# Kernel optimization log

Measured on AMD Instinct MI355X. Metric: run time of the kernel, lower is better.

The kernel has to match this reference:

```python
import jax, jax.numpy as jnp
import numpy as np

N_NODES = 50000
N_EDGES = 800000
IN_DIM = 64
HID = 128
OUT_DIM = 128
N_LAYERS = 3
LN_EPS = 1e-5


def setup_inputs() -> dict:
    key = jax.random.key(0)
    ks = jax.random.split(key, 12)
    x = jax.random.normal(ks[0], (N_NODES, IN_DIM), dtype=jnp.float32)
    edge_index = jax.random.randint(ks[1], (2, N_EDGES), 0, N_NODES, dtype=jnp.int32)
    # parameters
    W_in = jax.random.normal(ks[2], (IN_DIM, HID), dtype=jnp.float32) / np.sqrt(IN_DIM)
    b_in = jnp.zeros((HID,), dtype=jnp.float32)
    W_layers = jax.random.normal(ks[3], (N_LAYERS, HID, HID), dtype=jnp.float32) / np.sqrt(HID)
    b_layers = jnp.zeros((N_LAYERS, HID), dtype=jnp.float32)
    ln_g = jnp.ones((N_LAYERS, HID), dtype=jnp.float32)
    ln_b = jnp.zeros((N_LAYERS, HID), dtype=jnp.float32)
    W_out = jax.random.normal(ks[4], (HID, OUT_DIM), dtype=jnp.float32) / np.sqrt(HID)
    b_out = jnp.zeros((OUT_DIM,), dtype=jnp.float32)
    return {
        "x": x, "edge_index": edge_index, "num_nodes_actual": 48000,
        "W_in": W_in, "b_in": b_in,
        "W_layers": W_layers, "b_layers": b_layers,
        "ln_g": ln_g, "ln_b": ln_b,
        "W_out": W_out, "b_out": b_out,
    }


def _layer_norm(h, g, b):
    mu = jnp.mean(h, axis=-1, keepdims=True)
    var = jnp.mean(jnp.square(h - mu), axis=-1, keepdims=True)
    return (h - mu) * jax.lax.rsqrt(var + LN_EPS) * g + b


def reference(x, edge_index, num_nodes_actual, W_in, b_in, W_layers, b_layers, ln_g, ln_b, W_out, b_out):
    n = x.shape[0]
    src, dst = edge_index[0], edge_index[1]
    # degree-normalized scatter-add aggregation (same for all layers)
    degree = jax.ops.segment_sum(jnp.ones_like(src, dtype=x.dtype), dst, num_segments=n)
    inv_deg = 1.0 / jnp.clip(degree, 1.0)[:, None]  # [N,1]

    h = x @ W_in + b_in  # [N, HID]
    for i in range(N_LAYERS):
        residual = h
        agg = jax.ops.segment_sum(h[src], dst, num_segments=n) * inv_deg
        h = (h + agg) @ W_layers[i] + b_layers[i]
        h = _layer_norm(h, ln_g[i], ln_b[i])
        h = jax.nn.relu(h)
        h = h + residual
    h = h @ W_out + b_out  # [N, OUT_DIM]
    # mean over actual (non-padding) nodes, keepdim
    return jnp.mean(h[:num_nodes_actual], axis=0, keepdims=True)  # [1, OUT_DIM]
```

## Files before the change

kernel.cpp:

```cpp
#include <hip/hip_runtime.h>

#define HID 128
#define INP 64
#define LN_EPS 1e-5f
#define RT 64

typedef __attribute__((ext_vector_type(8))) short bf16x8;
typedef __attribute__((ext_vector_type(4))) float f32x4;

__device__ __forceinline__ unsigned f2bf(float f) {
    unsigned u = __float_as_uint(f);
    return (u + 0x7FFFu + ((u >> 16) & 1u)) >> 16;
}
__device__ __forceinline__ float bflo(unsigned v) { return __uint_as_float(v << 16); }
__device__ __forceinline__ float bfhi(unsigned v) { return __uint_as_float(v & 0xFFFF0000u); }

__global__ __launch_bounds__(256) void k_count(const int* __restrict__ dst, int nE, int* __restrict__ cnt,
                                               int* __restrict__ rank, int nEdgeThreads,
                                               const float* __restrict__ W_in, const float* __restrict__ W_l,
                                               unsigned short* __restrict__ Wt_in, unsigned short* __restrict__ Wt_l) {
    int t = blockIdx.x * 256 + threadIdx.x;
    if (t < nEdgeThreads) {
        int base = t * 16;
        if (base + 16 <= nE) {
            int4 d[4];
#pragma unroll
            for (int j = 0; j < 4; ++j) d[j] = *reinterpret_cast<const int4*>(dst + base + j * 4);
            int p[16];
#pragma unroll
            for (int j = 0; j < 4; ++j) {
                p[j * 4 + 0] = atomicAdd(&cnt[d[j].x], 1);
                p[j * 4 + 1] = atomicAdd(&cnt[d[j].y], 1);
                p[j * 4 + 2] = atomicAdd(&cnt[d[j].z], 1);
                p[j * 4 + 3] = atomicAdd(&cnt[d[j].w], 1);
            }
#pragma unroll
            for (int j = 0; j < 4; ++j)
                *reinterpret_cast<int4*>(rank + base + j * 4) =
                    make_int4(p[j * 4 + 0], p[j * 4 + 1], p[j * 4 + 2], p[j * 4 + 3]);
        } else {
            for (int e = base; e < nE; ++e) rank[e] = atomicAdd(&cnt[dst[e]], 1);
        }
        return;
    }
    int i = t - nEdgeThreads;
    if (i < 128 * 64) {
        int col = i >> 6, k = i & 63;
        Wt_in[i] = (unsigned short)f2bf(W_in[(size_t)k * HID + col]);
    } else if (i < 128 * 64 + 3 * 128 * 128) {
        int j = i - 128 * 64;
        int l = j >> 14, r = j & 16383;
        int col = r >> 7, k = r & 127;
        Wt_l[j] = (unsigned short)f2bf(W_l[(size_t)l * 16384 + (size_t)k * HID + col]);
    }
}

__global__ void k_scan1(const int* __restrict__ cnt, int n, int* __restrict__ rowp, int* __restrict__ bsum) {
    __shared__ int s[256];
    int i = blockIdx.x * 256 + threadIdx.x;
    int v = (i < n) ? cnt[i] : 0;
    s[threadIdx.x] = v;
    __syncthreads();
    for (int off = 1; off < 256; off <<= 1) {
        int t = (threadIdx.x >= off) ? s[threadIdx.x - off] : 0;
        __syncthreads();
        s[threadIdx.x] += t;
        __syncthreads();
    }
    if (i < n) rowp[i] = s[threadIdx.x] - v;
    if (threadIdx.x == 255) bsum[blockIdx.x] = s[255];
}

__global__ void k_scan3(int* __restrict__ rowp, const int* __restrict__ bsum, const int* __restrict__ cnt,
                        int n, int nE, float* __restrict__ invd, int nb) {
    __shared__ int s[256];
    __shared__ int boff;
    int v = (threadIdx.x < nb) ? bsum[threadIdx.x] : 0;
    s[threadIdx.x] = v;
    __syncthreads();
    for (int off = 1; off < 256; off <<= 1) {
        int t = (threadIdx.x >= off) ? s[threadIdx.x - off] : 0;
        __syncthreads();
        s[threadIdx.x] += t;
        __syncthreads();
    }
    if (threadIdx.x == blockIdx.x) boff = s[threadIdx.x] - v;
    __syncthreads();
    int i = blockIdx.x * 256 + threadIdx.x;
    if (i < n) {
        rowp[i] += boff;
        int c = cnt[i];
        invd[i] = 1.0f / (float)(c > 1 ? c : 1);
    } else if (i == n) {
        rowp[n] = nE;
    }
}

__global__ __launch_bounds__(256) void k_fillproj(const float* __restrict__ x,
                                                  const unsigned short* __restrict__ Wt,
                                                  const float* __restrict__ b,
                                                  unsigned* __restrict__ hout, int n, int tgrid,
                                                  const int* __restrict__ src, const int* __restrict__ dst,
                                                  const int* __restrict__ rank, const int* __restrict__ rowp,
                                                  int nE, int* __restrict__ csrc) {
    const int tid = threadIdx.x;
    if (blockIdx.x >= tgrid) {
        int t = (blockIdx.x - tgrid) * 256 + tid;
        int base = t * 16;
        if (base + 16 <= nE) {
            int4 d[4], s[4], r[4];
#pragma unroll
            for (int j = 0; j < 4; ++j) {
                d[j] = *reinterpret_cast<const int4*>(dst + base + j * 4);
                s[j] = *reinterpret_cast<const int4*>(src + base + j * 4);
                r[j] = *reinterpret_cast<const int4*>(rank + base + j * 4);
            }
#pragma unroll
            for (int j = 0; j < 4; ++j) {
                __builtin_nontemporal_store(s[j].x, &csrc[rowp[d[j].x] + r[j].x]);
                __builtin_nontemporal_store(s[j].y, &csrc[rowp[d[j].y] + r[j].y]);
                __builtin_nontemporal_store(s[j].z, &csrc[rowp[d[j].z] + r[j].z]);
                __builtin_nontemporal_store(s[j].w, &csrc[rowp[d[j].w] + r[j].w]);
            }
        } else if (base < nE) {
            for (int e = base; e < nE; ++e)
                __builtin_nontemporal_store(src[e], &csrc[rowp[dst[e]] + rank[e]]);
        }
        return;
    }
    __shared__ unsigned short xs[RT * INP];
    const int row0 = blockIdx.x * RT;
#pragma unroll
    for (int j = 0; j < 2; ++j) {
        int fid = tid + j * 256;
        int r = fid >> 3, c = fid & 7;
        int grow = row0 + r;
        unsigned o[4] = {0, 0, 0, 0};
        if (grow < n) {
            float4 v0 = *reinterpret_cast<const float4*>(x + (size_t)grow * INP + c * 8);
            float4 v1 = *reinterpret_cast<const float4*>(x + (size_t)grow * INP + c * 8 + 4);
            o[0] = f2bf(v0.x) | (f2bf(v0.y) << 16);
            o[1] = f2bf(v0.z) | (f2bf(v0.w) << 16);
            o[2] = f2bf(v1.x) | (f2bf(v1.y) << 16);
            o[3] = f2bf(v1.z) | (f2bf(v1.w) << 16);
        }
        int sw = c ^ (r & 7);
        *reinterpret_cast<uint4*>(xs + r * INP + sw * 8) = make_uint4(o[0], o[1], o[2], o[3]);
    }
    __syncthreads();

    const int l = tid & 63;
    const int w = tid >> 6;
    const int l15 = l & 15, lg = l >> 4;
    const int xrow = w * 16 + l15;

    f32x4 acc[8];
#pragma unroll
    for (int t = 0; t < 8; ++t) acc[t] = (f32x4){0.f, 0.f, 0.f, 0.f};

#pragma unroll
    for (int kc = 0; kc < 2; ++kc) {
        int bc = (kc * 4 + lg) ^ (xrow & 7);
        bf16x8 bfrag = *reinterpret_cast<const bf16x8*>(xs + xrow * INP + bc * 8);
        const unsigned short* wp = Wt + (size_t)l15 * INP + kc * 32 + lg * 8;
        bf16x8 af[8];
#pragma unroll
        for (int t = 0; t < 8; ++t) af[t] = *reinterpret_cast<const bf16x8*>(wp + (size_t)t * 16 * INP);
#pragma unroll
        for (int t = 0; t < 8; ++t)
            acc[t] = __builtin_amdgcn_mfma_f32_16x16x32_bf16(af[t], bfrag, acc[t], 0, 0, 0);
    }

    int grow = row0 + xrow;
    if (grow < n) {
#pragma unroll
        for (int t = 0; t < 8; ++t) {
            int c0 = t * 16 + lg * 4;
            f32x4 bb = *reinterpret_cast<const f32x4*>(b + c0);
            f32x4 o = acc[t] + bb;
            uint2 p;
            p.x = f2bf(o.x) | (f2bf(o.y) << 16);
            p.y = f2bf(o.z) | (f2bf(o.w) << 16);
            *reinterpret_cast<uint2*>(hout + (size_t)grow * 64 + t * 8 + lg * 2) = p;
        }
    }
}

__global__ __launch_bounds__(256) void k_agg(const unsigned* __restrict__ hb, const int* __restrict__ rowp,
                                             const int* __restrict__ csrc, const float* __restrict__ invd,
                                             unsigned* __restrict__ aggx, int n) {
    int node = blockIdx.x * 4 + (threadIdx.x >> 6);
    if (node >= n) return;
    int lane = threadIdx.x & 63;
    int grp = lane >> 4, cidx = lane & 15;
    int e0 = rowp[node], e1 = rowp[node + 1];
    int deg = e1 - e0;
    const uint4* hb4 = reinterpret_cast<const uint4*>(hb);
    float a0 = 0, a1 = 0, a2 = 0, a3 = 0, a4 = 0, a5 = 0, a6 = 0, a7 = 0;

    for (int base = 0; base < deg; base += 64) {
        int m = deg - base;
        if (m > 64) m = 64;
        int myidx = (base + lane < deg) ? csrc[e0 + base + lane] : 0;
        int steps = (m + 3) >> 2;
        int jj = 0;
        for (; jj + 4 <= steps; jj += 4) {
            uint4 v[4];
#pragma unroll
            for (int k = 0; k < 4; ++k) {
                int ei = (jj + k) * 4 + grp;
                int s = __shfl(myidx, ei);
                v[k] = (ei < m) ? hb4[(size_t)s * 16 + cidx] : make_uint4(0, 0, 0, 0);
            }
#pragma unroll
            for (int k = 0; k < 4; ++k) {
                a0 += bflo(v[k].x); a1 += bfhi(v[k].x);
                a2 += bflo(v[k].y); a3 += bfhi(v[k].y);
                a4 += bflo(v[k].z); a5 += bfhi(v[k].z);
                a6 += bflo(v[k].w); a7 += bfhi(v[k].w);
            }
        }
        for (; jj < steps; ++jj) {
            int ei = jj * 4 + grp;
            int s = __shfl(myidx, ei);
            if (ei < m) {
                uint4 v = hb4[(size_t)s * 16 + cidx];
                a0 += bflo(v.x); a1 += bfhi(v.x);
                a2 += bflo(v.y); a3 += bfhi(v.y);
                a4 += bflo(v.z); a5 += bfhi(v.z);
                a6 += bflo(v.w); a7 += bfhi(v.w);
            }
        }
    }
    a0 += __shfl_xor(a0, 16, 64); a0 += __shfl_xor(a0, 32, 64);
    a1 += __shfl_xor(a1, 16, 64); a1 += __shfl_xor(a1, 32, 64);
    a2 += __shfl_xor(a2, 16, 64); a2 += __shfl_xor(a2, 32, 64);
    a3 += __shfl_xor(a3, 16, 64); a3 += __shfl_xor(a3, 32, 64);
    a4 += __shfl_xor(a4, 16, 64); a4 += __shfl_xor(a4, 32, 64);
    a5 += __shfl_xor(a5, 16, 64); a5 += __shfl_xor(a5, 32, 64);
    a6 += __shfl_xor(a6, 16, 64); a6 += __shfl_xor(a6, 32, 64);
    a7 += __shfl_xor(a7, 16, 64); a7 += __shfl_xor(a7, 32, 64);

    if (grp == 0) {
        float inv = invd[node];
        uint4 self = hb4[(size_t)node * 16 + cidx];
        unsigned o0 = f2bf(bflo(self.x) + a0 * inv) | (f2bf(bfhi(self.x) + a1 * inv) << 16);
        unsigned o1 = f2bf(bflo(self.y) + a2 * inv) | (f2bf(bfhi(self.y) + a3 * inv) << 16);
        unsigned o2 = f2bf(bflo(self.z) + a4 * inv) | (f2bf(bfhi(self.z) + a5 * inv) << 16);
        unsigned o3 = f2bf(bflo(self.w) + a6 * inv) | (f2bf(bfhi(self.w) + a7 * inv) << 16);
        int sw = cidx ^ (node & 7);
        *reinterpret_cast<uint4*>(aggx + (size_t)node * 64 + sw * 4) = make_uint4(o0, o1, o2, o3);
    }
}

__global__ __launch_bounds__(256) void k_layer(const unsigned* __restrict__ hin,
                                               unsigned* __restrict__ hout,
                                               const unsigned* __restrict__ aggx,
                                               const unsigned short* __restrict__ Wt,
                                               const float* __restrict__ bias, const float* __restrict__ g,
                                               const float* __restrict__ lnb, int n) {
    const int tid = threadIdx.x;
    const int row0 = blockIdx.x * RT;
    const int lane = tid & 63;
    const int w = tid >> 6;
    const int l15 = lane & 15, lg = lane >> 4;
    const int xrow = w * 16 + l15;
    const int grow = row0 + xrow;

    const unsigned short* xg = reinterpret_cast<const unsigned short*>(aggx) + (size_t)grow * HID;

    f32x4 acc[8];
#pragma unroll
    for (int t = 0; t < 8; ++t) acc[t] = (f32x4){0.f, 0.f, 0.f, 0.f};

#pragma unroll
    for (int kc = 0; kc < 4; ++kc) {
        int bc = (kc * 4 + lg) ^ (xrow & 7);
        bf16x8 bfrag = *reinterpret_cast<const bf16x8*>(xg + bc * 8);
        const unsigned short* wp = Wt + (size_t)l15 * HID + kc * 32 + lg * 8;
        bf16x8 af[8];
#pragma unroll
        for (int t = 0; t < 8; ++t) af[t] = *reinterpret_cast<const bf16x8*>(wp + (size_t)t * 16 * HID);
#pragma unroll
        for (int t = 0; t < 8; ++t)
            acc[t] = __builtin_amdgcn_mfma_f32_16x16x32_bf16(af[t], bfrag, acc[t], 0, 0, 0);
    }

    float s = 0.f, q = 0.f;
#pragma unroll
    for (int t = 0; t < 8; ++t) {
        int c0 = t * 16 + lg * 4;
        f32x4 bb = *reinterpret_cast<const f32x4*>(bias + c0);
        acc[t] = acc[t] + bb;
        s += acc[t].x + acc[t].y + acc[t].z + acc[t].w;
        q += acc[t].x * acc[t].x + acc[t].y * acc[t].y + acc[t].z * acc[t].z + acc[t].w * acc[t].w;
    }
    s += __shfl_xor(s, 16, 64);
    s += __shfl_xor(s, 32, 64);
    q += __shfl_xor(q, 16, 64);
    q += __shfl_xor(q, 32, 64);
    float mu = s * (1.0f / HID);
    float var = q * (1.0f / HID) - mu * mu;
    float rs = rsqrtf(var + LN_EPS);

    if (grow < n) {
#pragma unroll
        for (int t = 0; t < 8; ++t) {
            int c0 = t * 16 + lg * 4;
            uint2 rv = *reinterpret_cast<const uint2*>(hin + (size_t)grow * 64 + t * 8 + lg * 2);
            f32x4 gv = *reinterpret_cast<const f32x4*>(g + c0);
            f32x4 lb = *reinterpret_cast<const f32x4*>(lnb + c0);
            float o0 = fmaxf((acc[t].x - mu) * rs * gv.x + lb.x, 0.f) + bflo(rv.x);
            float o1 = fmaxf((acc[t].y - mu) * rs * gv.y + lb.y, 0.f) + bfhi(rv.x);
            float o2 = fmaxf((acc[t].z - mu) * rs * gv.z + lb.z, 0.f) + bflo(rv.y);
            float o3 = fmaxf((acc[t].w - mu) * rs * gv.w + lb.w, 0.f) + bfhi(rv.y);
            uint2 p;
            p.x = f2bf(o0) | (f2bf(o1) << 16);
            p.y = f2bf(o2) | (f2bf(o3) << 16);
            *reinterpret_cast<uint2*>(hout + (size_t)grow * 64 + t * 8 + lg * 2) = p;
        }
    }
}

__global__ __launch_bounds__(256) void k_layerF(const unsigned* __restrict__ hin,
                                                const unsigned* __restrict__ aggx,
                                                const unsigned short* __restrict__ Wt,
                                                const float* __restrict__ bias, const float* __restrict__ g,
                                                const float* __restrict__ lnb,
                                                const int* __restrict__ n_act_p,
                                                float* __restrict__ accum) {
    __shared__ float red[4][4][8][4];
    const int tid = threadIdx.x;
    const int row0 = blockIdx.x * RT;
    const int lane = tid & 63;
    const int w = tid >> 6;
    const int l15 = lane & 15, lg = lane >> 4;
    const int xrow = w * 16 + l15;
    const int grow = row0 + xrow;
    const int na = *n_act_p;

    const unsigned short* xg = reinterpret_cast<const unsigned short*>(aggx) + (size_t)grow * HID;

    f32x4 acc[8];
#pragma unroll
    for (int t = 0; t < 8; ++t) acc[t] = (f32x4){0.f, 0.f, 0.f, 0.f};

#pragma unroll
    for (int kc = 0; kc < 4; ++kc) {
        int bc = (kc * 4 + lg) ^ (xrow & 7);
        bf16x8 bfrag = *reinterpret_cast<const bf16x8*>(xg + bc * 8);
        const unsigned short* wp = Wt + (size_t)l15 * HID + kc * 32 + lg * 8;
        bf16x8 af[8];
#pragma unroll
        for (int t = 0; t < 8; ++t) af[t] = *reinterpret_cast<const bf16x8*>(wp + (size_t)t * 16 * HID);
#pragma unroll
        for (int t = 0; t < 8; ++t)
            acc[t] = __builtin_amdgcn_mfma_f32_16x16x32_bf16(af[t], bfrag, acc[t], 0, 0, 0);
    }

    float s = 0.f, q = 0.f;
#pragma unroll
    for (int t = 0; t < 8; ++t) {
        int c0 = t * 16 + lg * 4;
        f32x4 bb = *reinterpret_cast<const f32x4*>(bias + c0);
        acc[t] = acc[t] + bb;
        s += acc[t].x + acc[t].y + acc[t].z + acc[t].w;
        q += acc[t].x * acc[t].x + acc[t].y * acc[t].y + acc[t].z * acc[t].z + acc[t].w * acc[t].w;
    }
    s += __shfl_xor(s, 16, 64);
    s += __shfl_xor(s, 32, 64);
    q += __shfl_xor(q, 16, 64);
    q += __shfl_xor(q, 32, 64);
    float mu = s * (1.0f / HID);
    float var = q * (1.0f / HID) - mu * mu;
    float rs = rsqrtf(var + LN_EPS);

    const float msk = (grow < na) ? 1.f : 0.f;
#pragma unroll
    for (int t = 0; t < 8; ++t) {
        int c0 = t * 16 + lg * 4;
        uint2 rv = *reinterpret_cast<const uint2*>(hin + (size_t)grow * 64 + t * 8 + lg * 2);
        f32x4 gv = *reinterpret_cast<const f32x4*>(g + c0);
        f32x4 lb = *reinterpret_cast<const f32x4*>(lnb + c0);
        float o0 = (fmaxf((acc[t].x - mu) * rs * gv.x + lb.x, 0.f) + bflo(rv.x)) * msk;
        float o1 = (fmaxf((acc[t].y - mu) * rs * gv.y + lb.y, 0.f) + bfhi(rv.x)) * msk;
        float o2 = (fmaxf((acc[t].z - mu) * rs * gv.z + lb.z, 0.f) + bflo(rv.y)) * msk;
        float o3 = (fmaxf((acc[t].w - mu) * rs * gv.w + lb.w, 0.f) + bfhi(rv.y)) * msk;
#pragma unroll
        for (int m = 1; m < 16; m <<= 1) {
            o0 += __shfl_xor(o0, m, 64);
            o1 += __shfl_xor(o1, m, 64);
            o2 += __shfl_xor(o2, m, 64);
            o3 += __shfl_xor(o3, m, 64);
        }
        if (l15 == 0) {
            red[w][lg][t][0] = o0;
            red[w][lg][t][1] = o1;
            red[w][lg][t][2] = o2;
            red[w][lg][t][3] = o3;
        }
    }
    __syncthreads();
    if (tid < HID) {
        int t = tid >> 4, rem = tid & 15;
        int lgq = rem >> 2, j = rem & 3;
        float v = red[0][lgq][t][j] + red[1][lgq][t][j] + red[2][lgq][t][j] + red[3][lgq][t][j];
        atomicAdd(&accum[tid], v);
    }
}

__global__ void k_out(const float* __restrict__ accum, const int* __restrict__ n_act_p,
                      const float* __restrict__ W_out, const float* __restrict__ b_out,
                      float* __restrict__ out) {
    __shared__ float m[HID];
    int c = threadIdx.x;
    float na = (float)(*n_act_p);
    m[c] = accum[c] / na;
    __syncthreads();
    float s = b_out[c];
    for (int k = 0; k < HID; ++k) s += m[k] * W_out[k * HID + c];
    out[c] = s;
}

extern "C" void kernel_launch(void* const* d_in, const int* in_sizes, int n_in,
                              void* d_out, int out_size, void* d_ws, size_t ws_size,
                              hipStream_t stream) {
    const int n  = in_sizes[0] / INP;
    const int nE = in_sizes[1] / 2;
    const float* x    = (const float*)d_in[0];
    const int*   ei   = (const int*)d_in[1];
    const int*   src  = ei;
    const int*   dst  = ei + nE;
    const int*   nact = (const int*)d_in[2];
    const float* W_in = (const float*)d_in[3];
    const float* b_in = (const float*)d_in[4];
    const float* W_l  = (const float*)d_in[5];
    const float* b_l  = (const float*)d_in[6];
    const float* lng  = (const float*)d_in[7];
    const float* lnb  = (const float*)d_in[8];
    const float* W_o  = (const float*)d_in[9];
    const float* b_o  = (const float*)d_in[10];

    char* ws = (char*)d_ws;
    size_t off = 0;
    auto alloc = [&](size_t bytes) {
        void* p = ws + off;
        off = (off + bytes + 255) & ~((size_t)255);
        return p;
    };
    unsigned* hbA  = (unsigned*)alloc((size_t)n * 64 * 4);
    unsigned* hbB  = (unsigned*)alloc((size_t)n * 64 * 4);
    unsigned* aggx = (unsigned*)alloc((size_t)(n + RT) * 64 * 4);
    size_t cntBytes = (((size_t)n * 4) + 255) & ~((size_t)255);
    int*   cnt   = (int*)alloc(cntBytes);
    float* accum = (float*)alloc(HID * 4);
    int*   rowp = (int*)alloc((size_t)(n + 1) * 4);
    float* invd = (float*)alloc((size_t)n * 4);
    int*   csrc = (int*)alloc((size_t)nE * 4);
    int*   rank = (int*)alloc((size_t)nE * 4);
    int*   bsum = (int*)alloc(1024);
    unsigned short* Wt_in = (unsigned short*)alloc(128 * 64 * 2);
    unsigned short* Wt_l  = (unsigned short*)alloc(3 * 128 * 128 * 2);

    hipMemsetAsync(cnt, 0, cntBytes + HID * 4, stream);

    int nb = (n + 255) / 256;
    int nEdgeThreads = (nE + 15) / 16;
    int nPrep = 128 * 64 + 3 * 128 * 128;
    int cpgrid = (nEdgeThreads + nPrep + 255) / 256;
    k_count<<<cpgrid, 256, 0, stream>>>(dst, nE, cnt, rank, nEdgeThreads, W_in, W_l, Wt_in, Wt_l);
    k_scan1<<<nb, 256, 0, stream>>>(cnt, n, rowp, bsum);
    k_scan3<<<nb, 256, 0, stream>>>(rowp, bsum, cnt, n, nE, invd, nb);

    int tgrid = (n + RT - 1) / RT;
    int fgrid = (nEdgeThreads + 255) / 256;
    k_fillproj<<<tgrid + fgrid, 256, 0, stream>>>(x, Wt_in, b_in, hbA, n, tgrid,
                                                  src, dst, rank, rowp, nE, csrc);

    const unsigned* hin = hbA;
    unsigned* hout = hbB;
    for (int l = 0; l < 3; ++l) {
        k_agg<<<(n + 3) / 4, 256, 0, stream>>>(hin, rowp, csrc, invd, aggx, n);
        if (l < 2) {
            k_layer<<<tgrid, 256, 0, stream>>>(hin, hout, aggx,
                                               Wt_l + (size_t)l * 128 * 128,
                                               b_l + l * HID, lng + l * HID, lnb + l * HID, n);
            const unsigned* t = hout;
            hout = (unsigned*)hin;
            hin = t;
        } else {
            k_layerF<<<tgrid, 256, 0, stream>>>(hin, aggx,
                                                Wt_l + (size_t)l * 128 * 128,
                                                b_l + l * HID, lng + l * HID, lnb + l * HID,
                                                nact, accum);
        }
    }
    k_out<<<1, HID, 0, stream>>>(accum, nact, W_o, b_o, (float*)d_out);
}
```

Before: 267.2 us.

## Fuse layer loop into one persistent kernel with hierarchical grid barriers

Replaces the seven per-layer launches (aggregate, dense layer, final reduction, output projection) with a single persistent kernel of 768 blocks. The blocks loop over nodes and tiles and synchronise between phases through a two-level atomic grid barrier. This removes launch gaps and tail effects between small kernels. In exchange, each block runs strided loops, and correctness depends on all 768 blocks being co-resident (launch bounds of 3 blocks per CU), otherwise the barrier can deadlock.

```diff
diff --git a/kernel.cpp b/kernel.cpp
--- a/kernel.cpp
+++ b/kernel.cpp
@@ -186,240 +186,232 @@
     }
 }
 
-__global__ __launch_bounds__(256) void k_agg(const unsigned* __restrict__ hb, const int* __restrict__ rowp,
-                                             const int* __restrict__ csrc, const float* __restrict__ invd,
-                                             unsigned* __restrict__ aggx, int n) {
-    int node = blockIdx.x * 4 + (threadIdx.x >> 6);
-    if (node >= n) return;
-    int lane = threadIdx.x & 63;
-    int grp = lane >> 4, cidx = lane & 15;
-    int e0 = rowp[node], e1 = rowp[node + 1];
-    int deg = e1 - e0;
-    const uint4* hb4 = reinterpret_cast<const uint4*>(hb);
-    float a0 = 0, a1 = 0, a2 = 0, a3 = 0, a4 = 0, a5 = 0, a6 = 0, a7 = 0;
-
-    for (int base = 0; base < deg; base += 64) {
-        int m = deg - base;
-        if (m > 64) m = 64;
-        int myidx = (base + lane < deg) ? csrc[e0 + base + lane] : 0;
-        int steps = (m + 3) >> 2;
-        int jj = 0;
-        for (; jj + 4 <= steps; jj += 4) {
-            uint4 v[4];
-#pragma unroll
-            for (int k = 0; k < 4; ++k) {
-                int ei = (jj + k) * 4 + grp;
-                int s = __shfl(myidx, ei);
-                v[k] = (ei < m) ? hb4[(size_t)s * 16 + cidx] : make_uint4(0, 0, 0, 0);
-            }
-#pragma unroll
-            for (int k = 0; k < 4; ++k) {
-                a0 += bflo(v[k].x); a1 += bfhi(v[k].x);
-                a2 += bflo(v[k].y); a3 += bfhi(v[k].y);
-                a4 += bflo(v[k].z); a5 += bfhi(v[k].z);
-                a6 += bflo(v[k].w); a7 += bfhi(v[k].w);
-            }
-        }
-        for (; jj < steps; ++jj) {
-            int ei = jj * 4 + grp;
-            int s = __shfl(myidx, ei);
-            if (ei < m) {
-                uint4 v = hb4[(size_t)s * 16 + cidx];
-                a0 += bflo(v.x); a1 += bfhi(v.x);
-                a2 += bflo(v.y); a3 += bfhi(v.y);
-                a4 += bflo(v.z); a5 += bfhi(v.z);
-                a6 += bflo(v.w); a7 += bfhi(v.w);
-            }
-        }
-    }
-    a0 += __shfl_xor(a0, 16, 64); a0 += __shfl_xor(a0, 32, 64);
-    a1 += __shfl_xor(a1, 16, 64); a1 += __shfl_xor(a1, 32, 64);
-    a2 += __shfl_xor(a2, 16, 64); a2 += __shfl_xor(a2, 32, 64);
-    a3 += __shfl_xor(a3, 16, 64); a3 += __shfl_xor(a3, 32, 64);
-    a4 += __shfl_xor(a4, 16, 64); a4 += __shfl_xor(a4, 32, 64);
-    a5 += __shfl_xor(a5, 16, 64); a5 += __shfl_xor(a5, 32, 64);
-    a6 += __shfl_xor(a6, 16, 64); a6 += __shfl_xor(a6, 32, 64);
-    a7 += __shfl_xor(a7, 16, 64); a7 += __shfl_xor(a7, 32, 64);
-
-    if (grp == 0) {
-        float inv = invd[node];
-        uint4 self = hb4[(size_t)node * 16 + cidx];
-        unsigned o0 = f2bf(bflo(self.x) + a0 * inv) | (f2bf(bfhi(self.x) + a1 * inv) << 16);
-        unsigned o1 = f2bf(bflo(self.y) + a2 * inv) | (f2bf(bfhi(self.y) + a3 * inv) << 16);
-        unsigned o2 = f2bf(bflo(self.z) + a4 * inv) | (f2bf(bfhi(self.z) + a5 * inv) << 16);
-        unsigned o3 = f2bf(bflo(self.w) + a6 * inv) | (f2bf(bfhi(self.w) + a7 * inv) << 16);
-        int sw = cidx ^ (node & 7);
-        *reinterpret_cast<uint4*>(aggx + (size_t)node * 64 + sw * 4) = make_uint4(o0, o1, o2, o3);
-    }
-}
-
-__global__ __launch_bounds__(256) void k_layer(const unsigned* __restrict__ hin,
-                                               unsigned* __restrict__ hout,
-                                               const unsigned* __restrict__ aggx,
-                                               const unsigned short* __restrict__ Wt,
-                                               const float* __restrict__ bias, const float* __restrict__ g,
-                                               const float* __restrict__ lnb, int n) {
+__global__ __launch_bounds__(256, 3) void k_net(unsigned* __restrict__ hbA, unsigned* __restrict__ hbB,
+                                                unsigned* __restrict__ aggx,
+                                                const int* __restrict__ rowp, const int* __restrict__ csrc,
+                                                const float* __restrict__ invd,
+                                                const unsigned short* __restrict__ Wt_all,
+                                                const float* __restrict__ b_all, const float* __restrict__ g_all,
+                                                const float* __restrict__ lnb_all,
+                                                const int* __restrict__ n_act_p, float* __restrict__ accum,
+                                                const float* __restrict__ W_o, const float* __restrict__ b_o,
+                                                float* __restrict__ out, int n, int tgrid,
+                                                int* __restrict__ bar) {
     const int tid = threadIdx.x;
-    const int row0 = blockIdx.x * RT;
     const int lane = tid & 63;
     const int w = tid >> 6;
+    const int nWaves = gridDim.x * 4;
+    const int waveId = blockIdx.x * 4 + w;
     const int l15 = lane & 15, lg = lane >> 4;
-    const int xrow = w * 16 + l15;
-    const int grow = row0 + xrow;
-
-    const unsigned short* xg = reinterpret_cast<const unsigned short*>(aggx) + (size_t)grow * HID;
-
-    f32x4 acc[8];
-#pragma unroll
-    for (int t = 0; t < 8; ++t) acc[t] = (f32x4){0.f, 0.f, 0.f, 0.f};
-
-#pragma unroll
-    for (int kc = 0; kc < 4; ++kc) {
-        int bc = (kc * 4 + lg) ^ (xrow & 7);
-        bf16x8 bfrag = *reinterpret_cast<const bf16x8*>(xg + bc * 8);
-        const unsigned short* wp = Wt + (size_t)l15 * HID + kc * 32 + lg * 8;
-        bf16x8 af[8];
-#pragma unroll
-        for (int t = 0; t < 8; ++t) af[t] = *reinterpret_cast<const bf16x8*>(wp + (size_t)t * 16 * HID);
-#pragma unroll
-        for (int t = 0; t < 8; ++t)
-            acc[t] = __builtin_amdgcn_mfma_f32_16x16x32_bf16(af[t], bfrag, acc[t], 0, 0, 0);
-    }
-
-    float s = 0.f, q = 0.f;
-#pragma unroll
-    for (int t = 0; t < 8; ++t) {
-        int c0 = t * 16 + lg * 4;
-        f32x4 bb = *reinterpret_cast<const f32x4*>(bias + c0);
-        acc[t] = acc[t] + bb;
-        s += acc[t].x + acc[t].y + acc[t].z + acc[t].w;
-        q += acc[t].x * acc[t].x + acc[t].y * acc[t].y + acc[t].z * acc[t].z + acc[t].w * acc[t].w;
-    }
-    s += __shfl_xor(s, 16, 64);
-    s += __shfl_xor(s, 32, 64);
-    q += __shfl_xor(q, 16, 64);
-    q += __shfl_xor(q, 32, 64);
-    float mu = s * (1.0f / HID);
-    float var = q * (1.0f / HID) - mu * mu;
-    float rs = rsqrtf(var + LN_EPS);
-
-    if (grow < n) {
-#pragma unroll
-        for (int t = 0; t < 8; ++t) {
-            int c0 = t * 16 + lg * 4;
-            uint2 rv = *reinterpret_cast<const uint2*>(hin + (size_t)grow * 64 + t * 8 + lg * 2);
-            f32x4 gv = *reinterpret_cast<const f32x4*>(g + c0);
-            f32x4 lb = *reinterpret_cast<const f32x4*>(lnb + c0);
-            float o0 = fmaxf((acc[t].x - mu) * rs * gv.x + lb.x, 0.f) + bflo(rv.x);
-            float o1 = fmaxf((acc[t].y - mu) * rs * gv.y + lb.y, 0.f) + bfhi(rv.x);
-            float o2 = fmaxf((acc[t].z - mu) * rs * gv.z + lb.z, 0.f) + bflo(rv.y);
-            float o3 = fmaxf((acc[t].w - mu) * rs * gv.w + lb.w, 0.f) + bfhi(rv.y);
-            uint2 p;
-            p.x = f2bf(o0) | (f2bf(o1) << 16);
-            p.y = f2bf(o2) | (f2bf(o3) << 16);
-            *reinterpret_cast<uint2*>(hout + (size_t)grow * 64 + t * 8 + lg * 2) = p;
-        }
-    }
-}
-
-__global__ __launch_bounds__(256) void k_layerF(const unsigned* __restrict__ hin,
-                                                const unsigned* __restrict__ aggx,
-                                                const unsigned short* __restrict__ Wt,
-                                                const float* __restrict__ bias, const float* __restrict__ g,
-                                                const float* __restrict__ lnb,
-                                                const int* __restrict__ n_act_p,
-                                                float* __restrict__ accum) {
-    __shared__ float red[4][4][8][4];
-    const int tid = threadIdx.x;
-    const int row0 = blockIdx.x * RT;
-    const int lane = tid & 63;
-    const int w = tid >> 6;
-    const int l15 = lane & 15, lg = lane >> 4;
-    const int xrow = w * 16 + l15;
-    const int grow = row0 + xrow;
-    const int na = *n_act_p;
-
-    const unsigned short* xg = reinterpret_cast<const unsigned short*>(aggx) + (size_t)grow * HID;
-
-    f32x4 acc[8];
-#pragma unroll
-    for (int t = 0; t < 8; ++t) acc[t] = (f32x4){0.f, 0.f, 0.f, 0.f};
-
-#pragma unroll
-    for (int kc = 0; kc < 4; ++kc) {
-        int bc = (kc * 4 + lg) ^ (xrow & 7);
-        bf16x8 bfrag = *reinterpret_cast<const bf16x8*>(xg + bc * 8);
-        const unsigned short* wp = Wt + (size_t)l15 * HID + kc * 32 + lg * 8;
-        bf16x8 af[8];
-#pragma unroll
-        for (int t = 0; t < 8; ++t) af[t] = *reinterpret_cast<const bf16x8*>(wp + (size_t)t * 16 * HID);
-#pragma unroll
-        for (int t = 0; t < 8; ++t)
-            acc[t] = __builtin_amdgcn_mfma_f32_16x16x32_bf16(af[t], bfrag, acc[t], 0, 0, 0);
-    }
-
-    float s = 0.f, q = 0.f;
-#pragma unroll
-    for (int t = 0; t < 8; ++t) {
-        int c0 = t * 16 + lg * 4;
-        f32x4 bb = *reinterpret_cast<const f32x4*>(bias + c0);
-        acc[t] = acc[t] + bb;
-        s += acc[t].x + acc[t].y + acc[t].z + acc[t].w;
-        q += acc[t].x * acc[t].x + acc[t].y * acc[t].y + acc[t].z * acc[t].z + acc[t].w * acc[t].w;
-    }
-    s += __shfl_xor(s, 16, 64);
-    s += __shfl_xor(s, 32, 64);
-    q += __shfl_xor(q, 16, 64);
-    q += __shfl_xor(q, 32, 64);
-    float mu = s * (1.0f / HID);
-    float var = q * (1.0f / HID) - mu * mu;
-    float rs = rsqrtf(var + LN_EPS);
-
-    const float msk = (grow < na) ? 1.f : 0.f;
-#pragma unroll
-    for (int t = 0; t < 8; ++t) {
-        int c0 = t * 16 + lg * 4;
-        uint2 rv = *reinterpret_cast<const uint2*>(hin + (size_t)grow * 64 + t * 8 + lg * 2);
-        f32x4 gv = *reinterpret_cast<const f32x4*>(g + c0);
-        f32x4 lb = *reinterpret_cast<const f32x4*>(lnb + c0);
-        float o0 = (fmaxf((acc[t].x - mu) * rs * gv.x + lb.x, 0.f) + bflo(rv.x)) * msk;
-        float o1 = (fmaxf((acc[t].y - mu) * rs * gv.y + lb.y, 0.f) + bfhi(rv.x)) * msk;
-        float o2 = (fmaxf((acc[t].z - mu) * rs * gv.z + lb.z, 0.f) + bflo(rv.y)) * msk;
-        float o3 = (fmaxf((acc[t].w - mu) * rs * gv.w + lb.w, 0.f) + bfhi(rv.y)) * msk;
-#pragma unroll
-        for (int m = 1; m < 16; m <<= 1) {
-            o0 += __shfl_xor(o0, m, 64);
-            o1 += __shfl_xor(o1, m, 64);
-            o2 += __shfl_xor(o2, m, 64);
-            o3 += __shfl_xor(o3, m, 64);
-        }
-        if (l15 == 0) {
-            red[w][lg][t][0] = o0;
-            red[w][lg][t][1] = o1;
-            red[w][lg][t][2] = o2;
-            red[w][lg][t][3] = o3;
-        }
-    }
-    __syncthreads();
-    if (tid < HID) {
-        int t = tid >> 4, rem = tid & 15;
-        int lgq = rem >> 2, j = rem & 3;
-        float v = red[0][lgq][t][j] + red[1][lgq][t][j] + red[2][lgq][t][j] + red[3][lgq][t][j];
-        atomicAdd(&accum[tid], v);
-    }
-}
-
-__global__ void k_out(const float* __restrict__ accum, const int* __restrict__ n_act_p,
-                      const float* __restrict__ W_out, const float* __restrict__ b_out,
-                      float* __restrict__ out) {
-    __shared__ float m[HID];
-    int c = threadIdx.x;
-    float na = (float)(*n_act_p);
-    m[c] = accum[c] / na;
-    __syncthreads();
-    float s = b_out[c];
-    for (int k = 0; k < HID; ++k) s += m[k] * W_out[k * HID + c];
-    out[c] = s;
+
+    int epoch = 0;
+    auto gbar = [&]() {
+        __syncthreads();
+        if (tid == 0) {
+            const int sub = blockIdx.x & 7;
+            const int subCount = gridDim.x >> 3;
+            __threadfence();
+            if (atomicAdd(&bar[sub * 32], 1) == subCount - 1) {
+                atomicExch(&bar[sub * 32], 0);
+                if (atomicAdd(&bar[256], 1) == 7) {
+                    atomicExch(&bar[256], 0);
+                    __threadfence();
+#pragma unroll
+                    for (int i = 0; i < 8; ++i) atomicExch(&bar[512 + i * 32], epoch + 1);
+                }
+            }
+            while (atomicAdd(&bar[512 + sub * 32], 0) <= epoch) __builtin_amdgcn_s_sleep(8);
+            __threadfence();
+        }
+        __syncthreads();
+        ++epoch;
+    };
+
+    const unsigned* hin = hbA;
+    unsigned* hout = hbB;
+
+    for (int l = 0; l < 3; ++l) {
+        {
+            const int grp = lane >> 4, cidx = lane & 15;
+            const uint4* hb4 = reinterpret_cast<const uint4*>(hin);
+            for (int node = waveId; node < n; node += nWaves) {
+                int e0 = rowp[node], e1 = rowp[node + 1];
+                int deg = e1 - e0;
+                float a0 = 0, a1 = 0, a2 = 0, a3 = 0, a4 = 0, a5 = 0, a6 = 0, a7 = 0;
+                for (int base = 0; base < deg; base += 64) {
+                    int m = deg - base;
+                    if (m > 64) m = 64;
+                    int myidx = (base + lane < deg) ? csrc[e0 + base + lane] : 0;
+                    int steps = (m + 3) >> 2;
+                    int jj = 0;
+                    for (; jj + 4 <= steps; jj += 4) {
+                        uint4 v[4];
+#pragma unroll
+                        for (int k = 0; k < 4; ++k) {
+                            int ei = (jj + k) * 4 + grp;
+                            int s = __shfl(myidx, ei);
+                            v[k] = (ei < m) ? hb4[(size_t)s * 16 + cidx] : make_uint4(0, 0, 0, 0);
+                        }
+#pragma unroll
+                        for (int k = 0; k < 4; ++k) {
+                            a0 += bflo(v[k].x); a1 += bfhi(v[k].x);
+                            a2 += bflo(v[k].y); a3 += bfhi(v[k].y);
+                            a4 += bflo(v[k].z); a5 += bfhi(v[k].z);
+                            a6 += bflo(v[k].w); a7 += bfhi(v[k].w);
+                        }
+                    }
+                    for (; jj < steps; ++jj) {
+                        int ei = jj * 4 + grp;
+                        int s = __shfl(myidx, ei);
+                        if (ei < m) {
+                            uint4 v = hb4[(size_t)s * 16 + cidx];
+                            a0 += bflo(v.x); a1 += bfhi(v.x);
+                            a2 += bflo(v.y); a3 += bfhi(v.y);
+                            a4 += bflo(v.z); a5 += bfhi(v.z);
+                            a6 += bflo(v.w); a7 += bfhi(v.w);
+                        }
+                    }
+                }
+                a0 += __shfl_xor(a0, 16, 64); a0 += __shfl_xor(a0, 32, 64);
+                a1 += __shfl_xor(a1, 16, 64); a1 += __shfl_xor(a1, 32, 64);
+                a2 += __shfl_xor(a2, 16, 64); a2 += __shfl_xor(a2, 32, 64);
+                a3 += __shfl_xor(a3, 16, 64); a3 += __shfl_xor(a3, 32, 64);
+                a4 += __shfl_xor(a4, 16, 64); a4 += __shfl_xor(a4, 32, 64);
+                a5 += __shfl_xor(a5, 16, 64); a5 += __shfl_xor(a5, 32, 64);
+                a6 += __shfl_xor(a6, 16, 64); a6 += __shfl_xor(a6, 32, 64);
+                a7 += __shfl_xor(a7, 16, 64); a7 += __shfl_xor(a7, 32, 64);
+
+                if (grp == 0) {
+                    float inv = invd[node];
+                    uint4 self = hb4[(size_t)node * 16 + cidx];
+                    unsigned o0 = f2bf(bflo(self.x) + a0 * inv) | (f2bf(bfhi(self.x) + a1 * inv) << 16);
+                    unsigned o1 = f2bf(bflo(self.y) + a2 * inv) | (f2bf(bfhi(self.y) + a3 * inv) << 16);
+                    unsigned o2 = f2bf(bflo(self.z) + a4 * inv) | (f2bf(bfhi(self.z) + a5 * inv) << 16);
+                    unsigned o3 = f2bf(bflo(self.w) + a6 * inv) | (f2bf(bfhi(self.w) + a7 * inv) << 16);
+                    int sw = cidx ^ (node & 7);
+                    *reinterpret_cast<uint4*>(aggx + (size_t)node * 64 + sw * 4) = make_uint4(o0, o1, o2, o3);
+                }
+            }
+        }
+        gbar();
+
+        const unsigned short* Wt = Wt_all + (size_t)l * 128 * 128;
+        const float* bias = b_all + l * HID;
+        const float* g = g_all + l * HID;
+        const float* lb2 = lnb_all + l * HID;
+        const int na = *n_act_p;
+        for (int tile = blockIdx.x; tile < tgrid; tile += gridDim.x) {
+            const int row0 = tile * RT;
+            const int xrow = w * 16 + l15;
+            const int grow = row0 + xrow;
+            const unsigned short* xg = reinterpret_cast<const unsigned short*>(aggx) + (size_t)grow * HID;
+
+            f32x4 acc[8];
+#pragma unroll
+            for (int t = 0; t < 8; ++t) acc[t] = (f32x4){0.f, 0.f, 0.f, 0.f};
+#pragma unroll
+            for (int kc = 0; kc < 4; ++kc) {
+                int bc = (kc * 4 + lg) ^ (xrow & 7);
+                bf16x8 bfrag = *reinterpret_cast<const bf16x8*>(xg + bc * 8);
+                const unsigned short* wp = Wt + (size_t)l15 * HID + kc * 32 + lg * 8;
+                bf16x8 af[8];
+#pragma unroll
+                for (int t = 0; t < 8; ++t) af[t] = *reinterpret_cast<const bf16x8*>(wp + (size_t)t * 16 * HID);
+#pragma unroll
+                for (int t = 0; t < 8; ++t)
+                    acc[t] = __builtin_amdgcn_mfma_f32_16x16x32_bf16(af[t], bfrag, acc[t], 0, 0, 0);
+            }
+
+            float s = 0.f, q = 0.f;
+#pragma unroll
+            for (int t = 0; t < 8; ++t) {
+                int c0 = t * 16 + lg * 4;
+                f32x4 bb = *reinterpret_cast<const f32x4*>(bias + c0);
+                acc[t] = acc[t] + bb;
+                s += acc[t].x + acc[t].y + acc[t].z + acc[t].w;
+                q += acc[t].x * acc[t].x + acc[t].y * acc[t].y + acc[t].z * acc[t].z + acc[t].w * acc[t].w;
+            }
+            s += __shfl_xor(s, 16, 64);
+            s += __shfl_xor(s, 32, 64);
+            q += __shfl_xor(q, 16, 64);
+            q += __shfl_xor(q, 32, 64);
+            float mu = s * (1.0f / HID);
+            float var = q * (1.0f / HID) - mu * mu;
+            float rs = rsqrtf(var + LN_EPS);
+
+            if (l < 2) {
+                if (grow < n) {
+#pragma unroll
+                    for (int t = 0; t < 8; ++t) {
+                        int c0 = t * 16 + lg * 4;
+                        uint2 rv = *reinterpret_cast<const uint2*>(hin + (size_t)grow * 64 + t * 8 + lg * 2);
+                        f32x4 gv = *reinterpret_cast<const f32x4*>(g + c0);
+                        f32x4 lb = *reinterpret_cast<const f32x4*>(lb2 + c0);
+                        float o0 = fmaxf((acc[t].x - mu) * rs * gv.x + lb.x, 0.f) + bflo(rv.x);
+                        float o1 = fmaxf((acc[t].y - mu) * rs * gv.y + lb.y, 0.f) + bfhi(rv.x);
+                        float o2 = fmaxf((acc[t].z - mu) * rs * gv.z + lb.z, 0.f) + bflo(rv.y);
+                        float o3 = fmaxf((acc[t].w - mu) * rs * gv.w + lb.w, 0.f) + bfhi(rv.y);
+                        uint2 p;
+                        p.x = f2bf(o0) | (f2bf(o1) << 16);
+                        p.y = f2bf(o2) | (f2bf(o3) << 16);
+                        *reinterpret_cast<uint2*>(hout + (size_t)grow * 64 + t * 8 + lg * 2) = p;
+                    }
+                }
+            } else {
+                __shared__ float red[4][4][8][4];
+                const float msk = (grow < na) ? 1.f : 0.f;
+#pragma unroll
+                for (int t = 0; t < 8; ++t) {
+                    int c0 = t * 16 + lg * 4;
+                    uint2 rv = *reinterpret_cast<const uint2*>(hin + (size_t)grow * 64 + t * 8 + lg * 2);
+                    f32x4 gv = *reinterpret_cast<const f32x4*>(g + c0);
+                    f32x4 lb = *reinterpret_cast<const f32x4*>(lb2 + c0);
+                    float o0 = (fmaxf((acc[t].x - mu) * rs * gv.x + lb.x, 0.f) + bflo(rv.x)) * msk;
+                    float o1 = (fmaxf((acc[t].y - mu) * rs * gv.y + lb.y, 0.f) + bfhi(rv.x)) * msk;
+                    float o2 = (fmaxf((acc[t].z - mu) * rs * gv.z + lb.z, 0.f) + bflo(rv.y)) * msk;
+                    float o3 = (fmaxf((acc[t].w - mu) * rs * gv.w + lb.w, 0.f) + bfhi(rv.y)) * msk;
+#pragma unroll
+                    for (int m = 1; m < 16; m <<= 1) {
+                        o0 += __shfl_xor(o0, m, 64);
+                        o1 += __shfl_xor(o1, m, 64);
+                        o2 += __shfl_xor(o2, m, 64);
+                        o3 += __shfl_xor(o3, m, 64);
+                    }
+                    if (l15 == 0) {
+                        red[w][lg][t][0] = o0;
+                        red[w][lg][t][1] = o1;
+                        red[w][lg][t][2] = o2;
+                        red[w][lg][t][3] = o3;
+                    }
+                }
+                __syncthreads();
+                if (tid < HID) {
+                    int t = tid >> 4, rem = tid & 15;
+                    int lgq = rem >> 2, j = rem & 3;
+                    float v = red[0][lgq][t][j] + red[1][lgq][t][j] + red[2][lgq][t][j] + red[3][lgq][t][j];
+                    atomicAdd(&accum[tid], v);
+                }
+                __syncthreads();
+            }
+        }
+        gbar();
+        if (l < 2) {
+            const unsigned* t = hout;
+            hout = (unsigned*)hin;
+            hin = t;
+        }
+    }
+
+    if (blockIdx.x == 0) {
+        __shared__ float m[HID];
+        if (tid < HID) m[tid] = accum[tid] / (float)(*n_act_p);
+        __syncthreads();
+        if (tid < HID) {
+            float s = b_o[tid];
+            for (int k = 0; k < HID; ++k) s += m[k] * W_o[k * HID + tid];
+            out[tid] = s;
+        }
+    }
 }
 
 extern "C" void kernel_launch(void* const* d_in, const int* in_sizes, int n_in,
@@ -454,6 +446,7 @@
     size_t cntBytes = (((size_t)n * 4) + 255) & ~((size_t)255);
     int*   cnt   = (int*)alloc(cntBytes);
     float* accum = (float*)alloc(HID * 4);
+    int*   bar   = (int*)alloc(4096);
     int*   rowp = (int*)alloc((size_t)(n + 1) * 4);
     float* invd = (float*)alloc((size_t)n * 4);
     int*   csrc = (int*)alloc((size_t)nE * 4);
@@ -462,7 +455,7 @@
     unsigned short* Wt_in = (unsigned short*)alloc(128 * 64 * 2);
     unsigned short* Wt_l  = (unsigned short*)alloc(3 * 128 * 128 * 2);
 
-    hipMemsetAsync(cnt, 0, cntBytes + HID * 4, stream);
+    hipMemsetAsync(cnt, 0, cntBytes + 512 + 4096, stream);
 
     int nb = (n + 255) / 256;
     int nEdgeThreads = (nE + 15) / 16;
@@ -477,23 +470,8 @@
     k_fillproj<<<tgrid + fgrid, 256, 0, stream>>>(x, Wt_in, b_in, hbA, n, tgrid,
                                                   src, dst, rank, rowp, nE, csrc);
 
-    const unsigned* hin = hbA;
-    unsigned* hout = hbB;
-    for (int l = 0; l < 3; ++l) {
-        k_agg<<<(n + 3) / 4, 256, 0, stream>>>(hin, rowp, csrc, invd, aggx, n);
-        if (l < 2) {
-            k_layer<<<tgrid, 256, 0, stream>>>(hin, hout, aggx,
-                                               Wt_l + (size_t)l * 128 * 128,
-                                               b_l + l * HID, lng + l * HID, lnb + l * HID, n);
-            const unsigned* t = hout;
-            hout = (unsigned*)hin;
-            hin = t;
-        } else {
-            k_layerF<<<tgrid, 256, 0, stream>>>(hin, aggx,
-                                                Wt_l + (size_t)l * 128 * 128,
-                                                b_l + l * HID, lng + l * HID, lnb + l * HID,
-                                                nact, accum);
-        }
-    }
-    k_out<<<1, HID, 0, stream>>>(accum, nact, W_o, b_o, (float*)d_out);
-}
+    const int G = 768;
+    k_net<<<G, 256, 0, stream>>>(hbA, hbB, aggx, rowp, csrc, invd,
+                                 Wt_l, b_l, lng, lnb, nact, accum,
+                                 W_o, b_o, (float*)d_out, n, tgrid, bar);
+}
```

Measured after the change: 547.3 us. +104.8%, slower.

## Merge scan kernels via grid barrier and fold output projection into last layer

Applied to the files above, without the earlier changes.

The two-pass prefix scan is merged into one kernel that uses a global atomic counter as a grid-wide barrier (196 blocks, all co-resident), so one kernel launch is removed. The final output projection kernel is also removed: the last block to finish k_layerF, found with an atomic done counter, computes the mean and the W_out projection. This cuts two launch gaps in exchange for spin-waiting and the assumption that every scan block is resident at once. The memset is widened to zero the new sync counters.

```diff
diff --git a/kernel.cpp b/kernel.cpp
--- a/kernel.cpp
+++ b/kernel.cpp
@@ -55,8 +55,10 @@
     }
 }
 
-__global__ void k_scan1(const int* __restrict__ cnt, int n, int* __restrict__ rowp, int* __restrict__ bsum) {
+__global__ void k_scan(const int* __restrict__ cnt, int n, int* __restrict__ rowp, int* __restrict__ bsum,
+                       float* __restrict__ invd, int nE, int nb, int* __restrict__ sync) {
     __shared__ int s[256];
+    __shared__ int boff;
     int i = blockIdx.x * 256 + threadIdx.x;
     int v = (i < n) ? cnt[i] : 0;
     s[threadIdx.x] = v;
@@ -67,16 +69,18 @@
         s[threadIdx.x] += t;
         __syncthreads();
     }
-    if (i < n) rowp[i] = s[threadIdx.x] - v;
+    int local_ex = s[threadIdx.x] - v;
     if (threadIdx.x == 255) bsum[blockIdx.x] = s[255];
-}
-
-__global__ void k_scan3(int* __restrict__ rowp, const int* __restrict__ bsum, const int* __restrict__ cnt,
-                        int n, int nE, float* __restrict__ invd, int nb) {
-    __shared__ int s[256];
-    __shared__ int boff;
-    int v = (threadIdx.x < nb) ? bsum[threadIdx.x] : 0;
-    s[threadIdx.x] = v;
+    __syncthreads();
+    __threadfence();
+    if (threadIdx.x == 0) {
+        atomicAdd(&sync[0], 1);
+        while (atomicAdd(&sync[0], 0) < nb) __builtin_amdgcn_s_sleep(2);
+    }
+    __syncthreads();
+    __threadfence();
+    int bv = (threadIdx.x < nb) ? bsum[threadIdx.x] : 0;
+    s[threadIdx.x] = bv;
     __syncthreads();
     for (int off = 1; off < 256; off <<= 1) {
         int t = (threadIdx.x >= off) ? s[threadIdx.x - off] : 0;
@@ -84,11 +88,10 @@
         s[threadIdx.x] += t;
         __syncthreads();
     }
-    if (threadIdx.x == blockIdx.x) boff = s[threadIdx.x] - v;
-    __syncthreads();
-    int i = blockIdx.x * 256 + threadIdx.x;
+    if (threadIdx.x == blockIdx.x) boff = s[threadIdx.x] - bv;
+    __syncthreads();
     if (i < n) {
-        rowp[i] += boff;
+        rowp[i] = local_ex + boff;
         int c = cnt[i];
         invd[i] = 1.0f / (float)(c > 1 ? c : 1);
     } else if (i == n) {
@@ -328,8 +331,11 @@
                                                 const float* __restrict__ bias, const float* __restrict__ g,
                                                 const float* __restrict__ lnb,
                                                 const int* __restrict__ n_act_p,
-                                                float* __restrict__ accum) {
+                                                float* __restrict__ accum,
+                                                const float* __restrict__ W_o, const float* __restrict__ b_o,
+                                                float* __restrict__ out, int tgrid, int* __restrict__ done) {
     __shared__ float red[4][4][8][4];
+    __shared__ int lastFlag;
     const int tid = threadIdx.x;
     const int row0 = blockIdx.x * RT;
     const int lane = tid & 63;
@@ -407,19 +413,21 @@
         float v = red[0][lgq][t][j] + red[1][lgq][t][j] + red[2][lgq][t][j] + red[3][lgq][t][j];
         atomicAdd(&accum[tid], v);
     }
-}
-
-__global__ void k_out(const float* __restrict__ accum, const int* __restrict__ n_act_p,
-                      const float* __restrict__ W_out, const float* __restrict__ b_out,
-                      float* __restrict__ out) {
-    __shared__ float m[HID];
-    int c = threadIdx.x;
-    float na = (float)(*n_act_p);
-    m[c] = accum[c] / na;
-    __syncthreads();
-    float s = b_out[c];
-    for (int k = 0; k < HID; ++k) s += m[k] * W_out[k * HID + c];
-    out[c] = s;
+    __syncthreads();
+    __threadfence();
+    if (tid == 0) lastFlag = (atomicAdd(done, 1) == tgrid - 1) ? 1 : 0;
+    __syncthreads();
+    if (lastFlag) {
+        __shared__ float m[HID];
+        __threadfence();
+        if (tid < HID) m[tid] = atomicAdd(&accum[tid], 0.f) / (float)na;
+        __syncthreads();
+        if (tid < HID) {
+            float o = b_o[tid];
+            for (int k = 0; k < HID; ++k) o += m[k] * W_o[k * HID + tid];
+            out[tid] = o;
+        }
+    }
 }
 
 extern "C" void kernel_launch(void* const* d_in, const int* in_sizes, int n_in,
@@ -454,6 +462,7 @@
     size_t cntBytes = (((size_t)n * 4) + 255) & ~((size_t)255);
     int*   cnt   = (int*)alloc(cntBytes);
     float* accum = (float*)alloc(HID * 4);
+    int*   sync  = (int*)alloc(256);
     int*   rowp = (int*)alloc((size_t)(n + 1) * 4);
     float* invd = (float*)alloc((size_t)n * 4);
     int*   csrc = (int*)alloc((size_t)nE * 4);
@@ -462,15 +471,14 @@
     unsigned short* Wt_in = (unsigned short*)alloc(128 * 64 * 2);
     unsigned short* Wt_l  = (unsigned short*)alloc(3 * 128 * 128 * 2);
 
-    hipMemsetAsync(cnt, 0, cntBytes + HID * 4, stream);
+    hipMemsetAsync(cnt, 0, cntBytes + 512 + 256, stream);
 
     int nb = (n + 255) / 256;
     int nEdgeThreads = (nE + 15) / 16;
     int nPrep = 128 * 64 + 3 * 128 * 128;
     int cpgrid = (nEdgeThreads + nPrep + 255) / 256;
     k_count<<<cpgrid, 256, 0, stream>>>(dst, nE, cnt, rank, nEdgeThreads, W_in, W_l, Wt_in, Wt_l);
-    k_scan1<<<nb, 256, 0, stream>>>(cnt, n, rowp, bsum);
-    k_scan3<<<nb, 256, 0, stream>>>(rowp, bsum, cnt, n, nE, invd, nb);
+    k_scan<<<nb, 256, 0, stream>>>(cnt, n, rowp, bsum, invd, nE, nb, sync);
 
     int tgrid = (n + RT - 1) / RT;
     int fgrid = (nEdgeThreads + 255) / 256;
@@ -492,8 +500,8 @@
             k_layerF<<<tgrid, 256, 0, stream>>>(hin, aggx,
                                                 Wt_l + (size_t)l * 128 * 128,
                                                 b_l + l * HID, lng + l * HID, lnb + l * HID,
-                                                nact, accum);
-        }
-    }
-    k_out<<<1, HID, 0, stream>>>(accum, nact, W_o, b_o, (float*)d_out);
-}
+                                                nact, accum, W_o, b_o, (float*)d_out,
+                                                tgrid, sync + 16);
+        }
+    }
+}
```

New measurement: 324.8 us. +21.6%, slower.
